# Kernel optimization log

Measured on AMD Instinct MI355X. Metric: run time of the kernel, lower is better.

The kernel has to match this reference:

```python
import jax, jax.numpy as jnp
import numpy as np

WIDTH = 768
HEAD = 64

def setup_inputs() -> dict:
    key = jax.random.key(0)
    ks = jax.random.split(key, 8)
    x = jax.random.normal(ks[0], (8, 2048, WIDTH), dtype=jnp.float32)
    mask = jax.random.randint(ks[1], (2048, 2048), 0, 2, dtype=jnp.int32)
    s = 1.0 / np.sqrt(WIDTH)
    Wq = jax.random.normal(ks[2], (WIDTH, HEAD), dtype=jnp.float32) * s
    Wk = jax.random.normal(ks[3], (WIDTH, HEAD), dtype=jnp.float32) * s
    Wv = jax.random.normal(ks[4], (WIDTH, HEAD), dtype=jnp.float32) * s
    bq = jax.random.normal(ks[5], (HEAD,), dtype=jnp.float32) * 0.01
    bk = jax.random.normal(ks[6], (HEAD,), dtype=jnp.float32) * 0.01
    bv = jax.random.normal(ks[7], (HEAD,), dtype=jnp.float32) * 0.01
    return {"x": x, "Wq": Wq, "bq": bq, "Wk": Wk, "bk": bk, "Wv": Wv, "bv": bv, "mask": mask}

def reference(x, Wq, bq, Wk, bk, Wv, bv, mask) -> jnp.ndarray:
    # x: [B, N, width]; projections -> [B, N, head]
    Q = jnp.einsum('bnw,wh->bnh', x, Wq) + bq
    K = jnp.einsum('bnw,wh->bnh', x, Wk) + bk
    V = jnp.einsum('bnw,wh->bnh', x, Wv) + bv
    scale = 1.0 / jnp.sqrt(jnp.asarray(Q.shape[-1], dtype=Q.dtype))
    scores = jnp.einsum('bqh,bkh->bqk', Q, K) * scale  # [B, N, N]
    scores = jnp.where(mask == 0, -jnp.inf, scores)
    attn = jax.nn.softmax(scores, axis=-1)
    return jnp.einsum('bqk,bkh->bqh', attn, V)
```

## Files before the change

kernel.cpp:

```cpp
#include <hip/hip_runtime.h>

typedef short  s8v   __attribute__((ext_vector_type(8)));
typedef float  f32x4 __attribute__((ext_vector_type(4)));

#define SEQ 2048
#define WID 768

__device__ __forceinline__ unsigned fbits(float f) {
    union { float f; unsigned u; } v; v.f = f; return v.u;
}
__device__ __forceinline__ float bitsf(unsigned u) {
    union { unsigned u; float f; } v; v.u = u; return v.f;
}
__device__ __forceinline__ unsigned short f2b(float f) {
    unsigned u = fbits(f);
    return (unsigned short)((u + 0x7FFFu + ((u >> 16) & 1u)) >> 16);
}
__device__ __forceinline__ unsigned packRNE(float a, float b) {
    unsigned ta = fbits(a) + 0x7FFFu + ((fbits(a) >> 16) & 1u);
    unsigned tb = fbits(b) + 0x7FFFu + ((fbits(b) >> 16) & 1u);
    return __builtin_amdgcn_perm(tb, ta, 0x07060302u);
}
__device__ __forceinline__ unsigned packTRUNC(float a, float b) {
    return __builtin_amdgcn_perm(fbits(b), fbits(a), 0x07060302u);
}
__device__ __forceinline__ f32x4 zero4() { f32x4 z = {0.f, 0.f, 0.f, 0.f}; return z; }

__device__ __forceinline__ void async16(const unsigned short* g, unsigned short* l) {
    __builtin_amdgcn_global_load_lds(
        (const __attribute__((address_space(1))) unsigned int*)g,
        (__attribute__((address_space(3))) unsigned int*)l, 16, 0, 0);
}
__device__ __forceinline__ void async16f(const float* g, float* l) {
    __builtin_amdgcn_global_load_lds(
        (const __attribute__((address_space(1))) unsigned int*)g,
        (__attribute__((address_space(3))) unsigned int*)l, 16, 0, 0);
}

__global__ __launch_bounds__(256) void prep_kernel(
    const int* __restrict__ mask,
    const float* __restrict__ Wq, const float* __restrict__ Wk, const float* __restrict__ Wv,
    unsigned* __restrict__ PM, unsigned short* __restrict__ Wt)
{
    const int tid = threadIdx.x;
    const int blk = blockIdx.x;
    if (blk < 512) {
        const int gid  = blk * 4 + (tid >> 6);
        const int lane = tid & 63, quad = lane >> 4, c = lane & 15;
        const int qb = gid >> 5, kb = gid & 31;
        unsigned w = 0;
        #pragma unroll
        for (int mt = 0; mt < 2; ++mt)
            #pragma unroll
            for (int i = 0; i < 4; ++i) {
                const int q = qb * 32 + mt * 16 + quad * 4 + i;
                const int4 mm = *(const int4*)&mask[(size_t)q * SEQ + kb * 64 + 4 * c];
                if (mm.x) w |= 1u << (mt * 16 + i * 4 + 0);
                if (mm.y) w |= 1u << (mt * 16 + i * 4 + 1);
                if (mm.z) w |= 1u << (mt * 16 + i * 4 + 2);
                if (mm.w) w |= 1u << (mt * 16 + i * 4 + 3);
            }
        PM[(size_t)gid * 64 + lane] = w;
    } else {
        const int cid = (blk - 512) * 256 + tid;
        const int mat = cid / 12288;
        const int rem = cid - mat * 12288;
        const int k = rem >> 4, c4 = rem & 15;
        const float* Wm = (mat == 0) ? Wq : (mat == 1) ? Wk : Wv;
        float4 w = *(const float4*)&Wm[(size_t)k * 64 + c4 * 4];
        float wv4[4] = {w.x, w.y, w.z, w.w};
        #pragma unroll
        for (int j = 0; j < 4; ++j)
            Wt[(size_t)(mat * 64 + c4 * 4 + j) * WID + k] = f2b(wv4[j]);
    }
}

__global__ __launch_bounds__(256, 4) void qkv_proj_kernel(
    const float* __restrict__ x, const unsigned short* __restrict__ Wt,
    const float* __restrict__ bq, const float* __restrict__ bk, const float* __restrict__ bv,
    unsigned short* __restrict__ QF, unsigned short* __restrict__ KF,
    unsigned short* __restrict__ VF)
{
    __shared__ __align__(16) unsigned char SMEM[49152];
    float (*Xs)[WID]           = (float(*)[WID])SMEM;
    unsigned short (*Xb)[776]  = (unsigned short(*)[776])(SMEM + 8192);
    unsigned short (*St)[208]  = (unsigned short(*)[208])SMEM;

    const int tid = threadIdx.x;
    const int wv = tid >> 6, lane = tid & 63, quad = lane >> 4, c = lane & 15;
    const int rowb = blockIdx.x * 16;
    const int c0w  = wv * 48;

    const float* xsrc = x + (size_t)rowb * WID;
    #pragma unroll
    for (int t = 0; t < 12; ++t) {
        const int d = wv * 12 + t;
        async16f(xsrc + d * 256 + lane * 4, (float*)SMEM + d * 256);
    }

    float bias[3];
    #pragma unroll
    for (int nt = 0; nt < 3; ++nt) {
        int col = c0w + nt * 16 + c;
        const float* B = (col < 64) ? bq : (col < 128) ? bk : bv;
        bias[nt] = B[col & 63];
    }
    __syncthreads();

    {
        const int r = tid >> 4, cc0 = (tid & 15) * 48;
        float4 f[12];
        #pragma unroll
        for (int j = 0; j < 12; ++j) f[j] = *(float4*)&Xs[r][cc0 + 4 * j];
        __syncthreads();
        #pragma unroll
        for (int j = 0; j < 6; ++j) {
            uint4 w;
            w.x = packRNE(f[2*j].x,   f[2*j].y);
            w.y = packRNE(f[2*j].z,   f[2*j].w);
            w.z = packRNE(f[2*j+1].x, f[2*j+1].y);
            w.w = packRNE(f[2*j+1].z, f[2*j+1].w);
            *(uint4*)&Xb[r][cc0 + 8 * j] = w;
        }
    }
    __syncthreads();

    f32x4 acc[3];
    #pragma unroll
    for (int nt = 0; nt < 3; ++nt) acc[nt] = zero4();

    uint4 pw[2][3];
    #pragma unroll
    for (int u = 0; u < 2; ++u)
        #pragma unroll
        for (int nt = 0; nt < 3; ++nt)
            pw[u][nt] = *(const uint4*)&Wt[(size_t)(c0w + nt * 16 + c) * WID + u * 32 + quad * 8];

    #pragma unroll
    for (int kc = 0; kc < 24; ++kc) {
        s8v af = *(const s8v*)&Xb[c][kc * 32 + quad * 8];
        union { uint4 u; s8v v; } bf[3];
        #pragma unroll
        for (int nt = 0; nt < 3; ++nt) bf[nt].u = pw[kc & 1][nt];
        if (kc + 2 < 24) {
            #pragma unroll
            for (int nt = 0; nt < 3; ++nt)
                pw[kc & 1][nt] = *(const uint4*)&Wt[(size_t)(c0w + nt * 16 + c) * WID + (kc + 2) * 32 + quad * 8];
        }
        #pragma unroll
        for (int nt = 0; nt < 3; ++nt)
            acc[nt] = __builtin_amdgcn_mfma_f32_16x16x32_bf16(af, bf[nt].v, acc[nt], 0, 0, 0);
    }

    #pragma unroll
    for (int nt = 0; nt < 3; ++nt)
        #pragma unroll
        for (int i = 0; i < 4; ++i)
            St[quad * 4 + i][c0w + nt * 16 + c] = f2b(acc[nt][i] + bias[nt]);
    __syncthreads();

    const int kb  = rowb >> 6;
    const int q0k = (rowb & 63) >> 2;
    const int ks0 = (rowb & 63) >> 5;
    const int qd0 = (rowb & 31) >> 3;

    if (tid < 128) {
        const int ks = tid >> 6, l = tid & 63, qd = l >> 4, cc = l & 15;
        uint4 v = *(uint4*)&St[cc][ks * 32 + qd * 8];
        *(uint4*)&QF[(((size_t)(rowb >> 4)) * 2 + ks) * 512 + (size_t)l * 8] = v;
    } else {
        const int u = tid - 128;
        const int ks = u >> 6, nt = (u >> 4) & 3, qd = (u >> 2) & 3, cc = u & 3;
        uint4 v = *(uint4*)&St[4 * cc + nt][64 + ks * 32 + qd * 8];
        *(uint4*)&KF[(((size_t)kb * 8 + ks * 4 + nt) * 64 + qd * 16 + q0k + cc) * 8] = v;
    }
    if (tid < 128) {
        const int d = tid >> 1, jj = tid & 1, qd = qd0 + jj;
        const int nt = d >> 4, cc = d & 15;
        unsigned short p[8];
        #pragma unroll
        for (int s = 0; s < 8; ++s) p[s] = St[jj * 8 + s][128 + d];
        uint4 w;
        w.x = (unsigned)p[0] | ((unsigned)p[1] << 16);
        w.y = (unsigned)p[2] | ((unsigned)p[3] << 16);
        w.z = (unsigned)p[4] | ((unsigned)p[5] << 16);
        w.w = (unsigned)p[6] | ((unsigned)p[7] << 16);
        *(uint4*)&VF[(((size_t)kb * 8 + ks0 * 4 + nt) * 64 + qd * 16 + cc) * 8] = w;
    }
}

__global__ __launch_bounds__(1024, 4) void attn_kernel(
    const unsigned short* __restrict__ QF, const unsigned short* __restrict__ KF,
    const unsigned short* __restrict__ VF, const unsigned* __restrict__ PM,
    float* __restrict__ out)
{
    __shared__ unsigned short KVk[2][4][4096];
    __shared__ __align__(16) unsigned char PsOb[36864];
    __shared__ float Lbuf[64];
    unsigned short (*Ps)[16][72] = (unsigned short(*)[16][72])PsOb;
    float (*Obuf)[68]            = (float(*)[68])PsOb;

    const int tid = threadIdx.x;
    const int wv = tid >> 6, lane = tid & 63, quad = lane >> 4, c = lane & 15;
    const int sl = wv & 3, qg = wv >> 2, mt = qg & 1;
    const int blk = blockIdx.x;
    const int bb = blk & 7, qt = blk >> 3;
    const size_t qrow0 = (size_t)bb * SEQ + qt * 64;

    if (tid < 64) Lbuf[tid] = 0.f;

    s8v qf[2];
    {
        const size_t qgrp = (size_t)bb * 128 + qt * 4 + qg;
        #pragma unroll
        for (int ks = 0; ks < 2; ++ks)
            qf[ks] = *(const s8v*)&QF[(qgrp * 2 + ks) * 512 + (size_t)lane * 8];
    }

    f32x4 O[4];
    float lro[4];
    #pragma unroll
    for (int nt = 0; nt < 4; ++nt) O[nt] = zero4();
    #pragma unroll
    for (int i = 0; i < 4; ++i) lro[i] = 0.f;

    {
        const size_t kbg = (size_t)bb * 32 + sl * 8;
        #pragma unroll
        for (int r = 0; r < 2; ++r) {
            const int cn = qg * 2 + r;
            async16(KF + kbg * 4096 + cn * 512 + lane * 8, &KVk[0][sl][cn * 512]);
        }
    }
    unsigned pm = PM[(size_t)((qt * 2 + (qg >> 1)) * 32 + sl * 8) * 64 + lane];

    for (int kt = 0; kt < 8; ++kt) {
        __syncthreads();

        if (kt < 7) {
            const size_t kbg = (size_t)bb * 32 + sl * 8 + kt + 1;
            #pragma unroll
            for (int r = 0; r < 2; ++r) {
                const int cn = qg * 2 + r;
                async16(KF + kbg * 4096 + cn * 512 + lane * 8, &KVk[(kt + 1) & 1][sl][cn * 512]);
            }
        }
        const unsigned pmN = (kt < 7)
            ? PM[(size_t)((qt * 2 + (qg >> 1)) * 32 + sl * 8 + kt + 1) * 64 + lane] : 0u;

        f32x4 S[4];
        #pragma unroll
        for (int nt = 0; nt < 4; ++nt) S[nt] = zero4();
        #pragma unroll
        for (int ks = 0; ks < 2; ++ks) {
            s8v kfr[4];
            #pragma unroll
            for (int nt = 0; nt < 4; ++nt)
                kfr[nt] = *(const s8v*)&KVk[kt & 1][sl][((ks * 4 + nt) * 64 + lane) * 8];
            #pragma unroll
            for (int nt = 0; nt < 4; ++nt)
                S[nt] = __builtin_amdgcn_mfma_f32_16x16x32_bf16(qf[ks], kfr[nt], S[nt], 0, 0, 0);
        }

        const size_t kbg = (size_t)bb * 32 + sl * 8 + kt;
        s8v vf[8];
        #pragma unroll
        for (int ks = 0; ks < 2; ++ks)
            #pragma unroll
            for (int nt = 0; nt < 4; ++nt)
                vf[ks * 4 + nt] = *(const s8v*)&VF[(kbg * 8 + ks * 4 + nt) * 512 + (size_t)lane * 8];

        const unsigned pmh = pm >> (mt * 16);
        #pragma unroll
        for (int i = 0; i < 4; ++i) {
            float p4[4];
            #pragma unroll
            for (int nt = 0; nt < 4; ++nt) {
                float e = exp2f(fmaf(S[nt][i], 0.18033688011112042f, -21.640425613334451f));
                p4[nt] = ((pmh >> (i * 4 + nt)) & 1u) ? e : 0.f;
            }
            unsigned u0 = packTRUNC(p4[0], p4[1]);
            unsigned u1 = packTRUNC(p4[2], p4[3]);
            lro[i] += bitsf(u0 << 16) + bitsf(u0 & 0xFFFF0000u)
                    + bitsf(u1 << 16) + bitsf(u1 & 0xFFFF0000u);
            *(uint2*)&Ps[wv][quad * 4 + i][4 * c] = make_uint2(u0, u1);
        }
        pm = pmN;

        #pragma unroll
        for (int ks = 0; ks < 2; ++ks) {
            s8v a = *(const s8v*)&Ps[wv][c][ks * 32 + quad * 8];
            #pragma unroll
            for (int nt = 0; nt < 4; ++nt)
                O[nt] = __builtin_amdgcn_mfma_f32_16x16x32_bf16(a, vf[ks * 4 + nt], O[nt], 0, 0, 0);
        }
    }

    __syncthreads();
    #pragma unroll
    for (int j = 0; j < 5; ++j) {
        int idx = tid + 1024 * j;
        if (idx < 64 * 68) ((float*)Obuf)[idx] = 0.f;
    }
    __syncthreads();
    #pragma unroll
    for (int i = 0; i < 4; ++i) {
        float l = lro[i];
        l += __shfl_xor(l, 1);
        l += __shfl_xor(l, 2);
        l += __shfl_xor(l, 4);
        l += __shfl_xor(l, 8);
        if (c == 0) atomicAdd(&Lbuf[qg * 16 + quad * 4 + i], l);
        #pragma unroll
        for (int nt = 0; nt < 4; ++nt)
            atomicAdd(&Obuf[qg * 16 + quad * 4 + i][nt * 16 + c], O[nt][i]);
    }
    __syncthreads();
    {
        const int r = tid >> 4, d4 = (tid & 15) * 4;
        const float invL = 1.0f / Lbuf[r];
        float4 v = *(float4*)&Obuf[r][d4];
        float4 o = make_float4(v.x * invL, v.y * invL, v.z * invL, v.w * invL);
        *(float4*)&out[(qrow0 + r) * 64 + d4] = o;
    }
}

extern "C" void kernel_launch(void* const* d_in, const int* in_sizes, int n_in,
                              void* d_out, int out_size, void* d_ws, size_t ws_size,
                              hipStream_t stream)
{
    const float* x    = (const float*)d_in[0];
    const float* Wq   = (const float*)d_in[1];
    const float* bq   = (const float*)d_in[2];
    const float* Wk   = (const float*)d_in[3];
    const float* bk   = (const float*)d_in[4];
    const float* Wv   = (const float*)d_in[5];
    const float* bv   = (const float*)d_in[6];
    const int*   mask = (const int*)d_in[7];
    float* out = (float*)d_out;

    unsigned short* QF = (unsigned short*)d_ws;
    unsigned short* KF = QF + (size_t)16384 * 64;
    unsigned short* VF = KF + (size_t)16384 * 64;
    unsigned short* Wt = VF + (size_t)16384 * 64;
    unsigned*       PM = (unsigned*)(Wt + (size_t)192 * WID);

    prep_kernel<<<656, 256, 0, stream>>>(mask, Wq, Wk, Wv, PM, Wt);
    qkv_proj_kernel<<<1024, 256, 0, stream>>>(x, Wt, bq, bk, bv, QF, KF, VF);
    attn_kernel<<<256, 1024, 0, stream>>>(QF, KF, VF, PM, out);
}
```

Baseline: 188.1 us.

## Drop LDS staging in projection and attention, load fragments directly from global

The weights are pre-packed into MFMA fragment order so the projection kernel can read x and W straight from global memory and convert x to bf16 in registers, with no LDS staging or barriers. The attention kernel is split into 1024 blocks of 256 threads, one 16-row query tile per block. Each wave reads its K and V fragments directly from global memory, replacing the async LDS double-buffering and the shared K tile. This removes LDS traffic and synchronisation, but gives up K reuse across query groups, so more global/L2 traffic is issued per block.

```diff
diff --git a/kernel.cpp b/kernel.cpp
--- a/kernel.cpp
+++ b/kernel.cpp
@@ -26,21 +26,10 @@
 }
 __device__ __forceinline__ f32x4 zero4() { f32x4 z = {0.f, 0.f, 0.f, 0.f}; return z; }
 
-__device__ __forceinline__ void async16(const unsigned short* g, unsigned short* l) {
-    __builtin_amdgcn_global_load_lds(
-        (const __attribute__((address_space(1))) unsigned int*)g,
-        (__attribute__((address_space(3))) unsigned int*)l, 16, 0, 0);
-}
-__device__ __forceinline__ void async16f(const float* g, float* l) {
-    __builtin_amdgcn_global_load_lds(
-        (const __attribute__((address_space(1))) unsigned int*)g,
-        (__attribute__((address_space(3))) unsigned int*)l, 16, 0, 0);
-}
-
-__global__ __launch_bounds__(256) void prep_kernel(
+__global__ __launch_bounds__(256) void convert_kernel(
     const int* __restrict__ mask,
     const float* __restrict__ Wq, const float* __restrict__ Wk, const float* __restrict__ Wv,
-    unsigned* __restrict__ PM, unsigned short* __restrict__ Wt)
+    unsigned* __restrict__ PM, unsigned short* __restrict__ WF)
 {
     const int tid = threadIdx.x;
     const int blk = blockIdx.x;
@@ -62,42 +51,37 @@
             }
         PM[(size_t)gid * 64 + lane] = w;
     } else {
-        const int cid = (blk - 512) * 256 + tid;
-        const int mat = cid / 12288;
-        const int rem = cid - mat * 12288;
-        const int k = rem >> 4, c4 = rem & 15;
+        const int s2 = (blk - 512) * 256 + tid;
+        const int chunk = s2 >> 6, l = s2 & 63;
+        const int ntg = chunk / 24, r = chunk - ntg * 24;
+        const int kc = r >> 1, h = r & 1;
+        const int mat = ntg >> 2;
+        const int col = (ntg & 3) * 16 + (l & 15);
+        const int k0 = kc * 64 + h * 32 + (l >> 4) * 8;
         const float* Wm = (mat == 0) ? Wq : (mat == 1) ? Wk : Wv;
-        float4 w = *(const float4*)&Wm[(size_t)k * 64 + c4 * 4];
-        float wv4[4] = {w.x, w.y, w.z, w.w};
-        #pragma unroll
-        for (int j = 0; j < 4; ++j)
-            Wt[(size_t)(mat * 64 + c4 * 4 + j) * WID + k] = f2b(wv4[j]);
+        float p[8];
+        #pragma unroll
+        for (int j = 0; j < 8; ++j) p[j] = Wm[(size_t)(k0 + j) * 64 + col];
+        uint4 w;
+        w.x = packRNE(p[0], p[1]); w.y = packRNE(p[2], p[3]);
+        w.z = packRNE(p[4], p[5]); w.w = packRNE(p[6], p[7]);
+        *(uint4*)&WF[(size_t)s2 * 8] = w;
     }
 }
 
 __global__ __launch_bounds__(256, 4) void qkv_proj_kernel(
-    const float* __restrict__ x, const unsigned short* __restrict__ Wt,
+    const float* __restrict__ x, const unsigned short* __restrict__ WF,
     const float* __restrict__ bq, const float* __restrict__ bk, const float* __restrict__ bv,
     unsigned short* __restrict__ QF, unsigned short* __restrict__ KF,
     unsigned short* __restrict__ VF)
 {
-    __shared__ __align__(16) unsigned char SMEM[49152];
-    float (*Xs)[WID]           = (float(*)[WID])SMEM;
-    unsigned short (*Xb)[776]  = (unsigned short(*)[776])(SMEM + 8192);
-    unsigned short (*St)[208]  = (unsigned short(*)[208])SMEM;
+    __shared__ unsigned short St[16][208];
 
     const int tid = threadIdx.x;
     const int wv = tid >> 6, lane = tid & 63, quad = lane >> 4, c = lane & 15;
     const int rowb = blockIdx.x * 16;
     const int c0w  = wv * 48;
 
-    const float* xsrc = x + (size_t)rowb * WID;
-    #pragma unroll
-    for (int t = 0; t < 12; ++t) {
-        const int d = wv * 12 + t;
-        async16f(xsrc + d * 256 + lane * 4, (float*)SMEM + d * 256);
-    }
-
     float bias[3];
     #pragma unroll
     for (int nt = 0; nt < 3; ++nt) {
@@ -105,51 +89,31 @@
         const float* B = (col < 64) ? bq : (col < 128) ? bk : bv;
         bias[nt] = B[col & 63];
     }
-    __syncthreads();
-
-    {
-        const int r = tid >> 4, cc0 = (tid & 15) * 48;
-        float4 f[12];
-        #pragma unroll
-        for (int j = 0; j < 12; ++j) f[j] = *(float4*)&Xs[r][cc0 + 4 * j];
-        __syncthreads();
-        #pragma unroll
-        for (int j = 0; j < 6; ++j) {
-            uint4 w;
-            w.x = packRNE(f[2*j].x,   f[2*j].y);
-            w.y = packRNE(f[2*j].z,   f[2*j].w);
-            w.z = packRNE(f[2*j+1].x, f[2*j+1].y);
-            w.w = packRNE(f[2*j+1].z, f[2*j+1].w);
-            *(uint4*)&Xb[r][cc0 + 8 * j] = w;
-        }
-    }
-    __syncthreads();
+
+    const float* xrow = x + (size_t)(rowb + c) * WID + quad * 8;
 
     f32x4 acc[3];
     #pragma unroll
     for (int nt = 0; nt < 3; ++nt) acc[nt] = zero4();
 
-    uint4 pw[2][3];
-    #pragma unroll
-    for (int u = 0; u < 2; ++u)
+    #pragma unroll
+    for (int kc = 0; kc < 24; ++kc) {
+        float4 f0 = *(const float4*)&xrow[kc * 32];
+        float4 f1 = *(const float4*)&xrow[kc * 32 + 4];
+        union { uint4 u; s8v v; } bf[3];
+        #pragma unroll
+        for (int nt = 0; nt < 3; ++nt) {
+            const int ntg = wv * 3 + nt;
+            bf[nt].u = *(const uint4*)&WF[(((size_t)ntg * 12 + (kc >> 1)) * 2 + (kc & 1)) * 512 + lane * 8];
+        }
+        union { uint4 u; s8v v; } af;
+        af.u.x = packRNE(f0.x, f0.y);
+        af.u.y = packRNE(f0.z, f0.w);
+        af.u.z = packRNE(f1.x, f1.y);
+        af.u.w = packRNE(f1.z, f1.w);
         #pragma unroll
         for (int nt = 0; nt < 3; ++nt)
-            pw[u][nt] = *(const uint4*)&Wt[(size_t)(c0w + nt * 16 + c) * WID + u * 32 + quad * 8];
-
-    #pragma unroll
-    for (int kc = 0; kc < 24; ++kc) {
-        s8v af = *(const s8v*)&Xb[c][kc * 32 + quad * 8];
-        union { uint4 u; s8v v; } bf[3];
-        #pragma unroll
-        for (int nt = 0; nt < 3; ++nt) bf[nt].u = pw[kc & 1][nt];
-        if (kc + 2 < 24) {
-            #pragma unroll
-            for (int nt = 0; nt < 3; ++nt)
-                pw[kc & 1][nt] = *(const uint4*)&Wt[(size_t)(c0w + nt * 16 + c) * WID + (kc + 2) * 32 + quad * 8];
-        }
-        #pragma unroll
-        for (int nt = 0; nt < 3; ++nt)
-            acc[nt] = __builtin_amdgcn_mfma_f32_16x16x32_bf16(af, bf[nt].v, acc[nt], 0, 0, 0);
+            acc[nt] = __builtin_amdgcn_mfma_f32_16x16x32_bf16(af.v, bf[nt].v, acc[nt], 0, 0, 0);
     }
 
     #pragma unroll
@@ -189,29 +153,31 @@
     }
 }
 
-__global__ __launch_bounds__(1024, 4) void attn_kernel(
+__global__ __launch_bounds__(256, 4) void attn_kernel(
     const unsigned short* __restrict__ QF, const unsigned short* __restrict__ KF,
     const unsigned short* __restrict__ VF, const unsigned* __restrict__ PM,
     float* __restrict__ out)
 {
-    __shared__ unsigned short KVk[2][4][4096];
-    __shared__ __align__(16) unsigned char PsOb[36864];
-    __shared__ float Lbuf[64];
-    unsigned short (*Ps)[16][72] = (unsigned short(*)[16][72])PsOb;
-    float (*Obuf)[68]            = (float(*)[68])PsOb;
+    __shared__ unsigned short Ps[4][16][72];
+    __shared__ float Obuf[16][68];
+    __shared__ float Lbuf[16];
 
     const int tid = threadIdx.x;
     const int wv = tid >> 6, lane = tid & 63, quad = lane >> 4, c = lane & 15;
-    const int sl = wv & 3, qg = wv >> 2, mt = qg & 1;
     const int blk = blockIdx.x;
-    const int bb = blk & 7, qt = blk >> 3;
-    const size_t qrow0 = (size_t)bb * SEQ + qt * 64;
-
-    if (tid < 64) Lbuf[tid] = 0.f;
+    const int bb = blk & 7, g = blk >> 3;
+    const int qb32 = g >> 1, mtq = g & 1;
+
+    #pragma unroll
+    for (int j = 0; j < 5; ++j) {
+        int idx = tid + 256 * j;
+        if (idx < 16 * 68) ((float*)Obuf)[idx] = 0.f;
+    }
+    if (tid < 16) Lbuf[tid] = 0.f;
 
     s8v qf[2];
     {
-        const size_t qgrp = (size_t)bb * 128 + qt * 4 + qg;
+        const size_t qgrp = (size_t)bb * 128 + g;
         #pragma unroll
         for (int ks = 0; ks < 2; ++ks)
             qf[ks] = *(const s8v*)&QF[(qgrp * 2 + ks) * 512 + (size_t)lane * 8];
@@ -224,53 +190,33 @@
     #pragma unroll
     for (int i = 0; i < 4; ++i) lro[i] = 0.f;
 
-    {
-        const size_t kbg = (size_t)bb * 32 + sl * 8;
-        #pragma unroll
-        for (int r = 0; r < 2; ++r) {
-            const int cn = qg * 2 + r;
-            async16(KF + kbg * 4096 + cn * 512 + lane * 8, &KVk[0][sl][cn * 512]);
-        }
-    }
-    unsigned pm = PM[(size_t)((qt * 2 + (qg >> 1)) * 32 + sl * 8) * 64 + lane];
-
+    #pragma unroll
     for (int kt = 0; kt < 8; ++kt) {
-        __syncthreads();
-
-        if (kt < 7) {
-            const size_t kbg = (size_t)bb * 32 + sl * 8 + kt + 1;
-            #pragma unroll
-            for (int r = 0; r < 2; ++r) {
-                const int cn = qg * 2 + r;
-                async16(KF + kbg * 4096 + cn * 512 + lane * 8, &KVk[(kt + 1) & 1][sl][cn * 512]);
-            }
-        }
-        const unsigned pmN = (kt < 7)
-            ? PM[(size_t)((qt * 2 + (qg >> 1)) * 32 + sl * 8 + kt + 1) * 64 + lane] : 0u;
+        const int kb = wv * 8 + kt;
+        const size_t kbg = (size_t)bb * 32 + kb;
+        const unsigned pm = PM[(size_t)(qb32 * 32 + kb) * 64 + lane];
+        const unsigned pmh = pm >> (mtq * 16);
 
         f32x4 S[4];
         #pragma unroll
         for (int nt = 0; nt < 4; ++nt) S[nt] = zero4();
-        #pragma unroll
-        for (int ks = 0; ks < 2; ++ks) {
-            s8v kfr[4];
-            #pragma unroll
-            for (int nt = 0; nt < 4; ++nt)
-                kfr[nt] = *(const s8v*)&KVk[kt & 1][sl][((ks * 4 + nt) * 64 + lane) * 8];
-            #pragma unroll
-            for (int nt = 0; nt < 4; ++nt)
-                S[nt] = __builtin_amdgcn_mfma_f32_16x16x32_bf16(qf[ks], kfr[nt], S[nt], 0, 0, 0);
-        }
-
-        const size_t kbg = (size_t)bb * 32 + sl * 8 + kt;
+        {
+            s8v kf[8];
+            #pragma unroll
+            for (int ch = 0; ch < 8; ++ch)
+                kf[ch] = *(const s8v*)&KF[(kbg * 8 + ch) * 512 + (size_t)lane * 8];
+            #pragma unroll
+            for (int ks = 0; ks < 2; ++ks)
+                #pragma unroll
+                for (int nt = 0; nt < 4; ++nt)
+                    S[nt] = __builtin_amdgcn_mfma_f32_16x16x32_bf16(qf[ks], kf[ks * 4 + nt], S[nt], 0, 0, 0);
+        }
+
         s8v vf[8];
         #pragma unroll
-        for (int ks = 0; ks < 2; ++ks)
-            #pragma unroll
-            for (int nt = 0; nt < 4; ++nt)
-                vf[ks * 4 + nt] = *(const s8v*)&VF[(kbg * 8 + ks * 4 + nt) * 512 + (size_t)lane * 8];
-
-        const unsigned pmh = pm >> (mt * 16);
+        for (int ch = 0; ch < 8; ++ch)
+            vf[ch] = *(const s8v*)&VF[(kbg * 8 + ch) * 512 + (size_t)lane * 8];
+
         #pragma unroll
         for (int i = 0; i < 4; ++i) {
             float p4[4];
@@ -285,7 +231,6 @@
                     + bitsf(u1 << 16) + bitsf(u1 & 0xFFFF0000u);
             *(uint2*)&Ps[wv][quad * 4 + i][4 * c] = make_uint2(u0, u1);
         }
-        pm = pmN;
 
         #pragma unroll
         for (int ks = 0; ks < 2; ++ks) {
@@ -296,12 +241,6 @@
         }
     }
 
-    __syncthreads();
-    #pragma unroll
-    for (int j = 0; j < 5; ++j) {
-        int idx = tid + 1024 * j;
-        if (idx < 64 * 68) ((float*)Obuf)[idx] = 0.f;
-    }
     __syncthreads();
     #pragma unroll
     for (int i = 0; i < 4; ++i) {
@@ -310,10 +249,10 @@
         l += __shfl_xor(l, 2);
         l += __shfl_xor(l, 4);
         l += __shfl_xor(l, 8);
-        if (c == 0) atomicAdd(&Lbuf[qg * 16 + quad * 4 + i], l);
+        if (c == 0) atomicAdd(&Lbuf[quad * 4 + i], l);
         #pragma unroll
         for (int nt = 0; nt < 4; ++nt)
-            atomicAdd(&Obuf[qg * 16 + quad * 4 + i][nt * 16 + c], O[nt][i]);
+            atomicAdd(&Obuf[quad * 4 + i][nt * 16 + c], O[nt][i]);
     }
     __syncthreads();
     {
@@ -321,7 +260,7 @@
         const float invL = 1.0f / Lbuf[r];
         float4 v = *(float4*)&Obuf[r][d4];
         float4 o = make_float4(v.x * invL, v.y * invL, v.z * invL, v.w * invL);
-        *(float4*)&out[(qrow0 + r) * 64 + d4] = o;
+        *(float4*)&out[((size_t)bb * SEQ + g * 16 + r) * 64 + d4] = o;
     }
 }
 
@@ -342,10 +281,10 @@
     unsigned short* QF = (unsigned short*)d_ws;
     unsigned short* KF = QF + (size_t)16384 * 64;
     unsigned short* VF = KF + (size_t)16384 * 64;
-    unsigned short* Wt = VF + (size_t)16384 * 64;
-    unsigned*       PM = (unsigned*)(Wt + (size_t)192 * WID);
-
-    prep_kernel<<<656, 256, 0, stream>>>(mask, Wq, Wk, Wv, PM, Wt);
-    qkv_proj_kernel<<<1024, 256, 0, stream>>>(x, Wt, bq, bk, bv, QF, KF, VF);
-    attn_kernel<<<256, 1024, 0, stream>>>(QF, KF, VF, PM, out);
-}
+    unsigned short* WF = VF + (size_t)16384 * 64;
+    unsigned*       PM = (unsigned*)(WF + (size_t)192 * WID);
+
+    convert_kernel<<<584, 256, 0, stream>>>(mask, Wq, Wk, Wv, PM, WF);
+    qkv_proj_kernel<<<1024, 256, 0, stream>>>(x, WF, bq, bk, bv, QF, KF, VF);
+    attn_kernel<<<1024, 256, 0, stream>>>(QF, KF, VF, PM, out);
+}
```

Result: faster. 174.4 us (-7.3%).
